# Optimization experiments

Measured on AMD Instinct MI355X. Metric: run time of the kernel, lower is better.

The kernel has to match this reference:

```python
import jax, jax.numpy as jnp
import numpy as np

B, S, C, NH = 4, 2048, 1024, 16
HD = C // NH


def setup_inputs() -> dict:
    key = jax.random.key(0)
    ks = jax.random.split(key, 8)
    w = lambda k, shape: (jax.random.normal(k, shape, dtype=jnp.float32) * 0.02)
    return {
        "x": jax.random.normal(ks[0], (B, S, C), dtype=jnp.float32),
        "y": jax.random.normal(ks[1], (B, S, C), dtype=jnp.float32),
        "mask": jnp.zeros((B, S), dtype=bool),  # True = padded key
        "Wq_w": w(ks[2], (C, C)),
        "Wq_b": jnp.zeros((C,), dtype=jnp.float32),
        "Wkv_w": w(ks[3], (2 * C, C)),
        "Wkv_b": jnp.zeros((2 * C,), dtype=jnp.float32),
        "Wo_w": w(ks[4], (C, C)),
        "Wo_b": jnp.zeros((C,), dtype=jnp.float32),
    }


def reference(x, y, mask, Wq_w, Wq_b, Wkv_w, Wkv_b, Wo_w, Wo_b):
    b, s, c = x.shape
    # projections (torch nn.Linear: x @ W.T + b)
    q = (x @ Wq_w.T + Wq_b).reshape(b, s, NH, HD).transpose(0, 2, 1, 3)  # bhsd
    kv = (y @ Wkv_w.T + Wkv_b).reshape(b, s, 2, NH, HD)
    k = kv[:, :, 0].transpose(0, 2, 1, 3)  # bhsd
    v = kv[:, :, 1].transpose(0, 2, 1, 3)  # bhsd
    # scores: [b, h, s_q, s_k]
    attn = jnp.einsum("bhqd,bhkd->bhqk", q, k) / np.sqrt(HD).astype(np.float32)
    causal = jnp.triu(jnp.ones((s, s), dtype=bool), 1)  # True above diagonal
    combined = causal[None, None] | mask[:, None, None, :]
    attn = jnp.where(combined, -jnp.inf, attn)
    attn = jax.nn.softmax(attn, axis=-1)
    out = jnp.einsum("bhqk,bhkd->bhqd", attn, v)
    out = out.transpose(0, 2, 1, 3).reshape(b, s, c)
    return out @ Wo_w.T + Wo_b
```

## Files before the change

kernel.cpp:

```cpp
#include <hip/hip_runtime.h>
#include <stdint.h>

#define B_  4
#define S_  2048
#define C_  1024
#define NH_ 16
#define HD_ 64
#define M_  (B_*S_)
#define NT_ (S_/64)
#define NKT 16

typedef __attribute__((ext_vector_type(8))) short bf16x8;
typedef __attribute__((ext_vector_type(4))) float f32x4;

typedef __attribute__((address_space(1))) const unsigned int gu32;
typedef __attribute__((address_space(3))) unsigned int lu32;

__device__ __forceinline__ void gload16(const void* g, void* l) {
    __builtin_amdgcn_global_load_lds((gu32*)g, (lu32*)l, 16, 0, 0);
}

__device__ __forceinline__ unsigned short f2bf(float f) {
    union { float f; unsigned u; } v; v.f = f;
    unsigned r = v.u + 0x7FFF + ((v.u >> 16) & 1);
    return (unsigned short)(r >> 16);
}

__global__ __launch_bounds__(256)
void cvt_all(const float4* __restrict__ x, const float4* __restrict__ y,
             const float4* __restrict__ wq, const float4* __restrict__ wkv,
             const float4* __restrict__ wo,
             uint4* __restrict__ xb, uint4* __restrict__ yb, uint4* __restrict__ wqb,
             uint4* __restrict__ wkvb, uint4* __restrict__ wob) {
    int i = blockIdx.x * 256 + threadIdx.x;
    const float4* src; uint4* dst; int off;
    if      (i < 1048576) { src = x;   dst = xb;   off = i; }
    else if (i < 2097152) { src = y;   dst = yb;   off = i - 1048576; }
    else if (i < 2228224) { src = wq;  dst = wqb;  off = i - 2097152; }
    else if (i < 2490368) { src = wkv; dst = wkvb; off = i - 2228224; }
    else                  { src = wo;  dst = wob;  off = i - 2490368; }
    float4 a = src[2*off], b = src[2*off+1];
    union { unsigned short s[8]; uint4 v; } u;
    u.s[0]=f2bf(a.x); u.s[1]=f2bf(a.y); u.s[2]=f2bf(a.z); u.s[3]=f2bf(a.w);
    u.s[4]=f2bf(b.x); u.s[5]=f2bf(b.y); u.s[6]=f2bf(b.z); u.s[7]=f2bf(b.w);
    dst[off] = u.v;
}


#define STAGE_A(mi, kb, db) do { \
    gload16(gA + (size_t)(mi)*64*1024 + (kb),           sh + (db)*32768 + (w*8 + (mi)*64)*64); \
    gload16(gA + ((size_t)(mi)*64 + 128)*1024 + (kb),   sh + (db)*32768 + (w*8 + 128 + (mi)*64)*64); \
} while (0)

#define STAGE_B(ni, kb, db) do { \
    gload16(gB + (size_t)(ni)*32*1024 + (kb),           sh + (db)*32768 + 16384 + ((w>>2)*64 + (w&3)*8 + (ni)*32)*64); \
    gload16(gB + ((size_t)(ni)*32 + 128)*1024 + (kb),   sh + (db)*32768 + 16384 + ((w>>2)*64 + (w&3)*8 + (ni)*32 + 128)*64); \
} while (0)

template<int MODE>
__device__ __forceinline__
void gemm256_body(const unsigned short* __restrict__ A, const unsigned short* __restrict__ Bt,
                  const float* __restrict__ bias,
                  unsigned short* __restrict__ out0, unsigned short* __restrict__ out1,
                  float* __restrict__ outf, int bx, int by, unsigned short* sh)
{
    const int t = threadIdx.x;
    const int lane = t & 63, w = t >> 6;
    const int quad = lane >> 4, l16 = lane & 15;
    const int wy = w >> 2, wx = w & 3;
    const int s7 = l16 & 7;
    const int colb = (quad ^ s7) << 3;
    const int c16 = (lane & 7) ^ (lane >> 3);

    const int rowA0 = by * 256;
    const int colB0 = bx * 256;

    const unsigned short* gA = A  + (size_t)(rowA0 + w*8 + (lane>>3))*1024 + c16*8;
    const unsigned short* gB = Bt + (size_t)(colB0 + (w>>2)*64 + (w&3)*8 + (lane>>3))*1024 + c16*8;

    f32x4 acc[2][2][4][2] = {};
    bf16x8 af[4][2], bfv[2][2][2];

    STAGE_A(0, 0, 0); STAGE_B(0, 0, 0); STAGE_B(1, 0, 0); STAGE_A(1, 0, 0);
    asm volatile("s_waitcnt vmcnt(4)" ::: "memory");
    __builtin_amdgcn_s_barrier();
    __builtin_amdgcn_sched_barrier(0);

    #pragma unroll 1
    for (int kt = 0; kt < NKT; ++kt) {
        const int cur = kt & 1;
        const int dstb = cur ^ 1;
        const unsigned short* Asb = sh + cur*32768;
        const unsigned short* Bsb = Asb + 16384;
        const int nkb = (kt + 1) * 64;
        const bool pre = (kt + 1 < NKT);

        #pragma unroll
        for (int p = 0; p < 4; ++p) {
            const int mi = p >> 1;
            const int ni = (p & 1) ^ mi;

            if (pre) {
                if      (p == 0) STAGE_A(0, nkb, dstb);
                else if (p == 1) STAGE_B(0, nkb, dstb);
                else if (p == 2) STAGE_B(1, nkb, dstb);
                else             STAGE_A(1, nkb, dstb);
            }
            if (p == 0) {
                #pragma unroll
                for (int mf = 0; mf < 4; ++mf) {
                    int idx = (wy*128 + mf*16 + l16)*64 + colb;
                    af[mf][0] = *(const bf16x8*)&Asb[idx];
                    af[mf][1] = *(const bf16x8*)&Asb[idx ^ 32];
                }
                #pragma unroll
                for (int nf = 0; nf < 2; ++nf) {
                    int idx = (wx*64 + nf*16 + l16)*64 + colb;
                    bfv[0][nf][0] = *(const bf16x8*)&Bsb[idx];
                    bfv[0][nf][1] = *(const bf16x8*)&Bsb[idx ^ 32];
                }
            } else if (p == 1) {
                #pragma unroll
                for (int nf = 0; nf < 2; ++nf) {
                    int idx = (wx*64 + 32 + nf*16 + l16)*64 + colb;
                    bfv[1][nf][0] = *(const bf16x8*)&Bsb[idx];
                    bfv[1][nf][1] = *(const bf16x8*)&Bsb[idx ^ 32];
                }
            } else if (p == 2) {
                #pragma unroll
                for (int mf = 0; mf < 4; ++mf) {
                    int idx = (wy*128 + 64 + mf*16 + l16)*64 + colb;
                    af[mf][0] = *(const bf16x8*)&Asb[idx];
                    af[mf][1] = *(const bf16x8*)&Asb[idx ^ 32];
                }
            }

            __builtin_amdgcn_s_barrier();
            __builtin_amdgcn_s_setprio(1);
            #pragma unroll
            for (int mf = 0; mf < 4; ++mf)
                #pragma unroll
                for (int nf = 0; nf < 2; ++nf) {
                    acc[mi][ni][mf][nf] = __builtin_amdgcn_mfma_f32_16x16x32_bf16(af[mf][0], bfv[ni][nf][0], acc[mi][ni][mf][nf], 0, 0, 0);
                    acc[mi][ni][mf][nf] = __builtin_amdgcn_mfma_f32_16x16x32_bf16(af[mf][1], bfv[ni][nf][1], acc[mi][ni][mf][nf], 0, 0, 0);
                }
            __builtin_amdgcn_s_setprio(0);

            if (p == 0) {
                if (pre) asm volatile("s_waitcnt vmcnt(2)" ::: "memory");
                else     asm volatile("s_waitcnt vmcnt(0)" ::: "memory");
            } else if (p == 3 && pre) {
                asm volatile("s_waitcnt vmcnt(4)" ::: "memory");
            }
            __builtin_amdgcn_s_barrier();
            __builtin_amdgcn_sched_barrier(0);
        }
    }

    const float QSCALE = 0.180336880111f;
    #pragma unroll
    for (int mi = 0; mi < 2; ++mi)
    #pragma unroll
    for (int ni = 0; ni < 2; ++ni)
    #pragma unroll
    for (int nf = 0; nf < 2; ++nf) {
        int gn = colB0 + wx*64 + ni*32 + nf*16 + l16;
        float bv = bias[gn];
        #pragma unroll
        for (int mf = 0; mf < 4; ++mf) {
            #pragma unroll
            for (int r = 0; r < 4; ++r) {
                int gm = rowA0 + wy*128 + mi*64 + mf*16 + quad*4 + r;
                float v = acc[mi][ni][mf][nf][r] + bv;
                if (MODE == 2) {
                    outf[(size_t)gm * 1024 + gn] = v;
                } else if (MODE == 0) {
                    v *= QSCALE;
                    int b = gm >> 11, s = gm & 2047;
                    int h = gn >> 6,  d = gn & 63;
                    out0[(((size_t)(b*NH_ + h)*S_ + s) << 6) + d] = f2bf(v);
                } else {
                    int b = gm >> 11, s = gm & 2047;
                    if (gn < C_) {
                        int h = gn >> 6, d = gn & 63;
                        out0[(((size_t)(b*NH_ + h)*S_ + s) << 6) + d] = f2bf(v);
                    } else {
                        int n2 = gn - C_;
                        int h = n2 >> 6, d = n2 & 63;
                        out1[((size_t)(b*NH_ + h)*HD_ + d)*S_ + s] = f2bf(v);
                    }
                }
            }
        }
    }
}

__global__ __launch_bounds__(512, 2)
void proj_fused256(const unsigned short* __restrict__ xb, const unsigned short* __restrict__ Wqb,
                   const float* __restrict__ Wq_b,
                   const unsigned short* __restrict__ yb, const unsigned short* __restrict__ Wkvb,
                   const float* __restrict__ Wkv_b,
                   unsigned short* __restrict__ Qg, unsigned short* __restrict__ Kg,
                   unsigned short* __restrict__ Vt)
{
    extern __shared__ unsigned short sh[];
    int id = blockIdx.x;
    if (id < 128) {
        gemm256_body<0>(xb, Wqb, Wq_b, Qg, nullptr, nullptr, id & 3, id >> 2, sh);
    } else {
        int j = id - 128;
        gemm256_body<1>(yb, Wkvb, Wkv_b, Kg, Vt, nullptr, j & 7, j >> 3, sh);
    }
}

__global__ __launch_bounds__(512, 2)
void gemm_oproj256(const unsigned short* __restrict__ A, const unsigned short* __restrict__ Bt,
                   const float* __restrict__ bias, float* __restrict__ outf)
{
    extern __shared__ unsigned short sh[];
    gemm256_body<2>(A, Bt, bias, nullptr, nullptr, outf, blockIdx.x & 3, blockIdx.x >> 2, sh);
}

__global__ __launch_bounds__(256, 4)
void attn_kernel(const unsigned short* __restrict__ Qg, const unsigned short* __restrict__ Kg,
                 const unsigned short* __restrict__ Vt, const unsigned char* __restrict__ maskp,
                 unsigned short* __restrict__ att)
{
    __shared__ unsigned short Pl[64*72];
    __shared__ float Lbuf[4][64];
    __shared__ float Linv[64];
    int t = threadIdx.x, lane = t & 63, w = t >> 6;
    int quad = lane >> 4, l16 = lane & 15;
    int bh = blockIdx.x, b = bh >> 4, h = bh & 15;
    int qi = blockIdx.y;

    const unsigned short* kbase = Kg + ((size_t)bh*S_ + w*16 + l16)*HD_ + quad*8;
    const unsigned short* vbase = Vt + ((size_t)bh*HD_ + w*16 + l16)*S_ + quad*8;
    int kp_row = w*16 + quad*4;
    const unsigned char* mbase = maskp + (size_t)b*S_ + kp_row;

    for (int half = 0; half < 2; ++half) {
        int qt = half ? (NT_ - 1 - qi) : qi;

        bf16x8 qf[4][2];
        #pragma unroll
        for (int m = 0; m < 4; ++m) {
            const unsigned short* qp = Qg + ((size_t)bh*S_ + qt*64 + m*16 + l16)*HD_;
            qf[m][0] = *reinterpret_cast<const bf16x8*>(qp + quad*8);
            qf[m][1] = *reinterpret_cast<const bf16x8*>(qp + 32 + quad*8);
        }
        f32x4 oacc[4] = {};
        float lsum[4] = {0.f, 0.f, 0.f, 0.f};

        bf16x8 kc0 = *reinterpret_cast<const bf16x8*>(kbase);
        bf16x8 kc1 = *reinterpret_cast<const bf16x8*>(kbase + 32);

        for (int kt = 0; kt <= qt; ++kt) {
            int ktn = (kt < qt) ? kt + 1 : kt;
            const unsigned short* kpn = kbase + (size_t)ktn*64*HD_;
            bf16x8 kn0 = *reinterpret_cast<const bf16x8*>(kpn);
            bf16x8 kn1 = *reinterpret_cast<const bf16x8*>(kpn + 32);
            const unsigned short* vp = vbase + kt*64;
            bf16x8 vc0 = *reinterpret_cast<const bf16x8*>(vp);
            bf16x8 vc1 = *reinterpret_cast<const bf16x8*>(vp + 32);

            unsigned m4 = *reinterpret_cast<const unsigned*>(mbase + kt*64);

            f32x4 sacc[4];
            #pragma unroll
            for (int m = 0; m < 4; ++m) {
                sacc[m] = __builtin_amdgcn_mfma_f32_16x16x32_bf16(kc0, qf[m][0], f32x4{}, 0, 0, 0);
                sacc[m] = __builtin_amdgcn_mfma_f32_16x16x32_bf16(kc1, qf[m][1], sacc[m], 0, 0, 0);
            }

            bool diag = (kt == qt);
            #pragma unroll
            for (int m = 0; m < 4; ++m) {
                float p[4];
                if (diag) {
                    #pragma unroll
                    for (int r = 0; r < 4; ++r) {
                        float s = sacc[m][r];
                        if (kp_row + r > m*16 + l16) s = -1e30f;
                        p[r] = __builtin_amdgcn_exp2f(s);
                    }
                } else {
                    #pragma unroll
                    for (int r = 0; r < 4; ++r)
                        p[r] = __builtin_amdgcn_exp2f(sacc[m][r]);
                }
                if (m4) {
                    #pragma unroll
                    for (int r = 0; r < 4; ++r)
                        if ((m4 >> (8*r)) & 0xFFu) p[r] = 0.f;
                }
                lsum[m] += (p[0] + p[1]) + (p[2] + p[3]);
                unsigned a01 = __builtin_amdgcn_perm(__float_as_uint(p[1]), __float_as_uint(p[0]), 0x07060302u);
                unsigned a23 = __builtin_amdgcn_perm(__float_as_uint(p[3]), __float_as_uint(p[2]), 0x07060302u);
                *reinterpret_cast<uint2*>(&Pl[(m*16 + l16)*72 + w*16 + quad*4]) = make_uint2(a01, a23);
            }
            __syncthreads();
            #pragma unroll
            for (int m = 0; m < 4; ++m) {
                bf16x8 pf0 = *reinterpret_cast<const bf16x8*>(&Pl[(m*16 + l16)*72 + quad*8]);
                bf16x8 pf1 = *reinterpret_cast<const bf16x8*>(&Pl[(m*16 + l16)*72 + 32 + quad*8]);
                oacc[m] = __builtin_amdgcn_mfma_f32_16x16x32_bf16(pf0, vc0, oacc[m], 0, 0, 0);
                oacc[m] = __builtin_amdgcn_mfma_f32_16x16x32_bf16(pf1, vc1, oacc[m], 0, 0, 0);
            }
            __syncthreads();
            kc0 = kn0; kc1 = kn1;
        }

        #pragma unroll
        for (int m = 0; m < 4; ++m) {
            lsum[m] += __shfl_xor(lsum[m], 16, 64);
            lsum[m] += __shfl_xor(lsum[m], 32, 64);
            Lbuf[w][m*16 + l16] = lsum[m];
        }
        __syncthreads();
        int q64 = t & 63;
        Linv[q64] = 1.0f / (Lbuf[0][q64] + Lbuf[1][q64] + Lbuf[2][q64] + Lbuf[3][q64]);
        __syncthreads();
        #pragma unroll
        for (int m = 0; m < 4; ++m) {
            #pragma unroll
            for (int r = 0; r < 4; ++r) {
                float iv = Linv[m*16 + quad*4 + r];
                int q = qt*64 + m*16 + quad*4 + r;
                att[((size_t)(b*S_ + q))*C_ + h*HD_ + w*16 + l16] = f2bf(oacc[m][r] * iv);
            }
        }
        __syncthreads();
    }
}

extern "C" void kernel_launch(void* const* d_in, const int* in_sizes, int n_in,
                              void* d_out, int out_size, void* d_ws, size_t ws_size,
                              hipStream_t stream) {
    const float* x     = (const float*)d_in[0];
    const float* y     = (const float*)d_in[1];
    const unsigned char* mask = (const unsigned char*)d_in[2];
    const float* Wq_w  = (const float*)d_in[3];
    const float* Wq_b  = (const float*)d_in[4];
    const float* Wkv_w = (const float*)d_in[5];
    const float* Wkv_b = (const float*)d_in[6];
    const float* Wo_w  = (const float*)d_in[7];
    const float* Wo_b  = (const float*)d_in[8];
    float* out = (float*)d_out;

    unsigned short* xb   = (unsigned short*)d_ws;
    unsigned short* yb   = xb   + (size_t)M_*C_;
    unsigned short* Wqb  = yb   + (size_t)M_*C_;
    unsigned short* Wkvb = Wqb  + (size_t)C_*C_;
    unsigned short* Wob  = Wkvb + (size_t)2*C_*C_;
    unsigned short* Qg   = Wob  + (size_t)C_*C_;
    unsigned short* Kg   = Qg   + (size_t)M_*C_;
    unsigned short* Vtg  = Kg   + (size_t)M_*C_;
    unsigned short* att  = xb;

    static bool once = []() {
        hipFuncSetAttribute((const void*)proj_fused256, hipFuncAttributeMaxDynamicSharedMemorySize, 131072);
        hipFuncSetAttribute((const void*)gemm_oproj256, hipFuncAttributeMaxDynamicSharedMemorySize, 131072);
        return true;
    }();
    (void)once;

    cvt_all<<<10240, 256, 0, stream>>>((const float4*)x, (const float4*)y,
        (const float4*)Wq_w, (const float4*)Wkv_w, (const float4*)Wo_w,
        (uint4*)xb, (uint4*)yb, (uint4*)Wqb, (uint4*)Wkvb, (uint4*)Wob);

    proj_fused256<<<384, 512, 131072, stream>>>(xb, Wqb, Wq_b, yb, Wkvb, Wkv_b, Qg, Kg, Vtg);
    attn_kernel<<<dim3(B_*NH_, NT_/2), 256, 0, stream>>>(Qg, Kg, Vtg, mask, att);
    gemm_oproj256<<<128, 512, 131072, stream>>>(att, Wob, Wo_b, out);
}
```

Before: 334.3 us.

## Prefetch GEMM tiles two k-steps ahead with quadrant-level buffer reuse

Reworks the 256x256 GEMM main loop so that global-to-LDS loads run up to two k-tiles ahead. Each quadrant of the double buffer is refilled for tile kt+2 as soon as its fragments have been read into registers. The four MFMA phases are reordered (00, 01, 11, 10) so that freed A/B halves can be overwritten early, and the vmcnt waits are adjusted to match. This is meant to hide more global-memory latency behind MFMA work without adding LDS. The cost is more complex wait-count bookkeeping, where one wrong count would race on the buffers.

```diff
diff --git a/kernel.cpp b/kernel.cpp
--- a/kernel.cpp
+++ b/kernel.cpp
@@ -57,6 +57,35 @@
     gload16(gB + ((size_t)(ni)*32 + 128)*1024 + (kb),   sh + (db)*32768 + 16384 + ((w>>2)*64 + (w&3)*8 + (ni)*32 + 128)*64); \
 } while (0)
 
+#define READ_A(half) do { \
+    _Pragma("unroll") \
+    for (int mf = 0; mf < 4; ++mf) { \
+        int idx = (wy*128 + (half)*64 + mf*16 + l16)*64 + colb; \
+        af[mf][0] = *(const bf16x8*)&Asb[idx]; \
+        af[mf][1] = *(const bf16x8*)&Asb[idx ^ 32]; \
+    } \
+} while (0)
+
+#define READ_B(half) do { \
+    _Pragma("unroll") \
+    for (int nf = 0; nf < 2; ++nf) { \
+        int idx = (wx*64 + (half)*32 + nf*16 + l16)*64 + colb; \
+        bfv[half][nf][0] = *(const bf16x8*)&Bsb[idx]; \
+        bfv[half][nf][1] = *(const bf16x8*)&Bsb[idx ^ 32]; \
+    } \
+} while (0)
+
+#define MFMA_Q(mi, ni) do { \
+    _Pragma("unroll") \
+    for (int mf = 0; mf < 4; ++mf) { \
+        _Pragma("unroll") \
+        for (int nf = 0; nf < 2; ++nf) { \
+            acc[mi][ni][mf][nf] = __builtin_amdgcn_mfma_f32_16x16x32_bf16(af[mf][0], bfv[ni][nf][0], acc[mi][ni][mf][nf], 0, 0, 0); \
+            acc[mi][ni][mf][nf] = __builtin_amdgcn_mfma_f32_16x16x32_bf16(af[mf][1], bfv[ni][nf][1], acc[mi][ni][mf][nf], 0, 0, 0); \
+        } \
+    } \
+} while (0)
+
 template<int MODE>
 __device__ __forceinline__
 void gemm256_body(const unsigned short* __restrict__ A, const unsigned short* __restrict__ Bt,
@@ -81,80 +110,65 @@
     f32x4 acc[2][2][4][2] = {};
     bf16x8 af[4][2], bfv[2][2][2];
 
-    STAGE_A(0, 0, 0); STAGE_B(0, 0, 0); STAGE_B(1, 0, 0); STAGE_A(1, 0, 0);
-    asm volatile("s_waitcnt vmcnt(4)" ::: "memory");
+    STAGE_A(0, 0, 0);
+    STAGE_B(1, 0, 0);
+    STAGE_B(0, 0, 0);
+    STAGE_A(1, 0, 0);
+    STAGE_A(0, 64, 1);
+    STAGE_B(1, 64, 1);
+    asm volatile("s_waitcnt vmcnt(6)" ::: "memory");
     __builtin_amdgcn_s_barrier();
     __builtin_amdgcn_sched_barrier(0);
 
     #pragma unroll 1
     for (int kt = 0; kt < NKT; ++kt) {
         const int cur = kt & 1;
-        const int dstb = cur ^ 1;
         const unsigned short* Asb = sh + cur*32768;
         const unsigned short* Bsb = Asb + 16384;
-        const int nkb = (kt + 1) * 64;
-        const bool pre = (kt + 1 < NKT);
-
-        #pragma unroll
-        for (int p = 0; p < 4; ++p) {
-            const int mi = p >> 1;
-            const int ni = (p & 1) ^ mi;
-
-            if (pre) {
-                if      (p == 0) STAGE_A(0, nkb, dstb);
-                else if (p == 1) STAGE_B(0, nkb, dstb);
-                else if (p == 2) STAGE_B(1, nkb, dstb);
-                else             STAGE_A(1, nkb, dstb);
-            }
-            if (p == 0) {
-                #pragma unroll
-                for (int mf = 0; mf < 4; ++mf) {
-                    int idx = (wy*128 + mf*16 + l16)*64 + colb;
-                    af[mf][0] = *(const bf16x8*)&Asb[idx];
-                    af[mf][1] = *(const bf16x8*)&Asb[idx ^ 32];
-                }
-                #pragma unroll
-                for (int nf = 0; nf < 2; ++nf) {
-                    int idx = (wx*64 + nf*16 + l16)*64 + colb;
-                    bfv[0][nf][0] = *(const bf16x8*)&Bsb[idx];
-                    bfv[0][nf][1] = *(const bf16x8*)&Bsb[idx ^ 32];
-                }
-            } else if (p == 1) {
-                #pragma unroll
-                for (int nf = 0; nf < 2; ++nf) {
-                    int idx = (wx*64 + 32 + nf*16 + l16)*64 + colb;
-                    bfv[1][nf][0] = *(const bf16x8*)&Bsb[idx];
-                    bfv[1][nf][1] = *(const bf16x8*)&Bsb[idx ^ 32];
-                }
-            } else if (p == 2) {
-                #pragma unroll
-                for (int mf = 0; mf < 4; ++mf) {
-                    int idx = (wy*128 + 64 + mf*16 + l16)*64 + colb;
-                    af[mf][0] = *(const bf16x8*)&Asb[idx];
-                    af[mf][1] = *(const bf16x8*)&Asb[idx ^ 32];
-                }
-            }
-
-            __builtin_amdgcn_s_barrier();
-            __builtin_amdgcn_s_setprio(1);
-            #pragma unroll
-            for (int mf = 0; mf < 4; ++mf)
-                #pragma unroll
-                for (int nf = 0; nf < 2; ++nf) {
-                    acc[mi][ni][mf][nf] = __builtin_amdgcn_mfma_f32_16x16x32_bf16(af[mf][0], bfv[ni][nf][0], acc[mi][ni][mf][nf], 0, 0, 0);
-                    acc[mi][ni][mf][nf] = __builtin_amdgcn_mfma_f32_16x16x32_bf16(af[mf][1], bfv[ni][nf][1], acc[mi][ni][mf][nf], 0, 0, 0);
-                }
-            __builtin_amdgcn_s_setprio(0);
-
-            if (p == 0) {
-                if (pre) asm volatile("s_waitcnt vmcnt(2)" ::: "memory");
-                else     asm volatile("s_waitcnt vmcnt(0)" ::: "memory");
-            } else if (p == 3 && pre) {
-                asm volatile("s_waitcnt vmcnt(4)" ::: "memory");
-            }
-            __builtin_amdgcn_s_barrier();
-            __builtin_amdgcn_sched_barrier(0);
-        }
+        const int kb1 = (kt + 1) * 64;
+        const int kb2 = (kt + 2) * 64;
+        const bool st1 = (kt + 1 < NKT);
+        const bool st2 = (kt + 2 < NKT);
+
+        if (st1) STAGE_B(0, kb1, cur ^ 1);
+        READ_A(0);
+        READ_B(0);
+        __builtin_amdgcn_s_barrier();
+        __builtin_amdgcn_s_setprio(1);
+        MFMA_Q(0, 0);
+        __builtin_amdgcn_s_setprio(0);
+        __builtin_amdgcn_s_barrier();
+        __builtin_amdgcn_sched_barrier(0);
+
+        if (st1) STAGE_A(1, kb1, cur ^ 1);
+        READ_B(1);
+        __builtin_amdgcn_s_barrier();
+        __builtin_amdgcn_s_setprio(1);
+        MFMA_Q(0, 1);
+        __builtin_amdgcn_s_setprio(0);
+        if (st1) asm volatile("s_waitcnt vmcnt(8)" ::: "memory");
+        else     asm volatile("s_waitcnt vmcnt(0)" ::: "memory");
+        __builtin_amdgcn_s_barrier();
+        __builtin_amdgcn_sched_barrier(0);
+
+        if (st2) STAGE_A(0, kb2, cur);
+        READ_A(1);
+        __builtin_amdgcn_s_barrier();
+        __builtin_amdgcn_s_setprio(1);
+        MFMA_Q(1, 1);
+        __builtin_amdgcn_s_setprio(0);
+        __builtin_amdgcn_s_barrier();
+        __builtin_amdgcn_sched_barrier(0);
+
+        if (st2) STAGE_B(1, kb2, cur);
+        __builtin_amdgcn_s_barrier();
+        __builtin_amdgcn_s_setprio(1);
+        MFMA_Q(1, 0);
+        __builtin_amdgcn_s_setprio(0);
+        if      (st2) asm volatile("s_waitcnt vmcnt(6)" ::: "memory");
+        else if (st1) asm volatile("s_waitcnt vmcnt(2)" ::: "memory");
+        __builtin_amdgcn_s_barrier();
+        __builtin_amdgcn_sched_barrier(0);
     }
 
     const float QSCALE = 0.180336880111f;
```

Result: no change. 333.3 us (-0.3%).
